# Kernel optimization log

Measured on AMD Instinct MI355X. Metric: run time of the kernel, lower is better.

## Reference

```python
import jax, jax.numpy as jnp
import numpy as np

STEPS = 100
RATE = 200
THR = 1.0
BETA = 0.0
SG_ALPHA = 2.0  # snntorch default ATan surrogate alpha


@jax.custom_vjp
def spike_fn(x):
    # heaviside spike with atan surrogate gradient (snntorch default)
    return (x > 0).astype(x.dtype)

def _spike_fwd(x):
    return spike_fn(x), x

def _spike_bwd(x, g):
    grad = (SG_ALPHA / 2.0) / (1.0 + (jnp.pi / 2.0 * SG_ALPHA * x) ** 2)
    return (g * grad,)

spike_fn.defvjp(_spike_fwd, _spike_bwd)


def conv2d(x, w):
    # x: [B,C,H,W], w: [O,I,K,K], VALID, stride 1, no bias
    return jax.lax.conv_general_dilated(
        x, w, window_strides=(1, 1), padding='VALID',
        dimension_numbers=('NCHW', 'OIHW', 'NCHW'))


def avg_pool2(x):
    s = jax.lax.reduce_window(x, 0.0, jax.lax.add, (1, 1, 2, 2), (1, 1, 2, 2), 'VALID')
    return s * 0.25


def lif(cur, mem):
    # snntorch Leaky, reset_mechanism='subtract'; reset signal is detached
    reset = jax.lax.stop_gradient((mem > THR).astype(cur.dtype))
    mem = BETA * mem + cur - reset * THR
    spk = spike_fn(mem - THR)
    return spk, mem


def setup_inputs() -> dict:
    key = jax.random.key(0)
    k1, k2, k3, k4 = jax.random.split(key, 4)
    B, C, H, W = 64, 3, 32, 32
    x = jax.random.uniform(k1, (B, C, H, W), dtype=jnp.float32)
    # kaiming-uniform-ish init scales (exact values irrelevant for correctness baseline)
    W_in = jax.random.normal(k2, (32, 3, 5, 5), dtype=jnp.float32) * 0.1
    W_h1 = jax.random.normal(k3, (64, 32, 5, 5), dtype=jnp.float32) * 0.05
    W_h2 = jax.random.normal(k4, (10, 1600), dtype=jnp.float32) * 0.02
    return {"x": x, "W_in": W_in, "W_h1": W_h1, "W_h2": W_h2}


def reference(x, W_in, W_h1, W_h2):
    B, C, H, W = x.shape
    K = W_in.shape[2]
    # poisson spike train: [steps, B, C, H, W]
    rescale = RATE / STEPS
    rand = jax.random.uniform(jax.random.key(1), (STEPS, B, C, H, W), dtype=x.dtype)
    spikes = (rand < x * rescale).astype(x.dtype)

    H1 = (H - K + 1) // 2; W1 = (W - K + 1) // 2           # after conv1+pool
    H2 = (H1 - K + 1) // 2; W2 = (W1 - K + 1) // 2          # after conv2+pool
    mem0 = (jnp.zeros((B, W_in.shape[0], H1, W1), x.dtype),
            jnp.zeros((B, W_h1.shape[0], H2, W2), x.dtype),
            jnp.zeros((B, W_h2.shape[0]), x.dtype))

    def step(carry, s):
        memin, memh1, memh2 = carry
        spkin, memin = lif(avg_pool2(conv2d(s, W_in)), memin)
        spkh1, memh1 = lif(avg_pool2(conv2d(spkin, W_h1)), memh1)
        flat = spkh1.reshape(spkh1.shape[0], -1)
        spkh2, memh2 = lif(flat @ W_h2.T, memh2)
        return (memin, memh1, memh2), (spkh2, memh2)

    _, (out_spikes, memh2_mem) = jax.lax.scan(step, mem0, spikes)
    return out_spikes, memh2_mem
```

## Files before the change

### kernel.cpp

```cpp
#include <hip/hip_runtime.h>
#include <stdint.h>


#define NSTEPS 100
#define NB 64
#define CAPF1 524288u
#define CAPF2 262144u

typedef short bf16x8 __attribute__((ext_vector_type(8)));
typedef float f32x4 __attribute__((ext_vector_type(4)));

__device__ __forceinline__ uint32_t rotl32(uint32_t v, uint32_t r) {
  return (v << r) | (v >> (32u - r));
}

__device__ __forceinline__ void threefry2x32(uint32_t k0, uint32_t k1,
                                             uint32_t& x0, uint32_t& x1) {
  uint32_t k2 = k0 ^ k1 ^ 0x1BD11BDAu;
  x0 += k0; x1 += k1;
#define TF_R(r) { x0 += x1; x1 = rotl32(x1, r); x1 ^= x0; }
  TF_R(13u) TF_R(15u) TF_R(26u) TF_R(6u)
  x0 += k1; x1 += k2 + 1u;
  TF_R(17u) TF_R(29u) TF_R(16u) TF_R(24u)
  x0 += k2; x1 += k0 + 2u;
  TF_R(13u) TF_R(15u) TF_R(26u) TF_R(6u)
  x0 += k0; x1 += k1 + 3u;
  TF_R(17u) TF_R(29u) TF_R(16u) TF_R(24u)
  x0 += k1; x1 += k2 + 4u;
  TF_R(13u) TF_R(15u) TF_R(26u) TF_R(6u)
  x0 += k2; x1 += k0 + 5u;
#undef TF_R
}

__device__ __forceinline__ double fold_pool_w(const float* W, int base, int pos) {
  int iy = pos / 6, ix = pos % 6;
  double w = 0.0;
  for (int dy = 0; dy < 2; ++dy) {
    int ky = iy - dy; if (ky < 0 || ky > 4) continue;
    for (int dx = 0; dx < 2; ++dx) {
      int kx = ix - dx; if (kx < 0 || kx > 4) continue;
      w += (double)W[base + ky * 5 + kx];
    }
  }
  return w;
}

__device__ __forceinline__ uint16_t f2bf(float x) {
  uint32_t u = __float_as_uint(x);
  uint32_t r = (u + 0x7fffu + ((u >> 16) & 1u)) >> 16;
  return (uint16_t)r;
}

__global__ __launch_bounds__(256) void prep_gen(const float* __restrict__ W_in,
                                                const float* __restrict__ W_h1,
                                                const float* __restrict__ x,
                                                double* __restrict__ W1R,
                                                double* __restrict__ W2R,
                                                uint16_t* __restrict__ WB1,
                                                uint16_t* __restrict__ WB2,
                                                float* __restrict__ EPS,
                                                uint32_t* __restrict__ cnt,
                                                uint32_t* __restrict__ rowm) {
  if (blockIdx.x >= 678) {
    int id = (blockIdx.x - 678) * 4 + (threadIdx.x >> 6);
    int lane = threadIdx.x & 63;
    int rp = id & 15, c = (id >> 4) % 3, tb = id / 48;
    int pix = rp * 64 + lane;
    int b = tb & 63;
    uint32_t i = (uint32_t)((tb * 3 + c) * 1024 + pix);
    uint32_t x0 = 0u, x1 = i;
    threefry2x32(0u, 1u, x0, x1);
    uint32_t bits = x0 ^ x1;
    float u = __uint_as_float((bits >> 9) | 0x3f800000u) - 1.0f;
    float xv = x[(b * 3 + c) * 1024 + pix];
    unsigned long long mask = __ballot(u < 2.0f * xv);
    if (lane == 0) ((unsigned long long*)rowm)[id] = mask;
    return;
  }
  if (blockIdx.x < 654) {
    int e = blockIdx.x * 256 + threadIdx.x;
    if (e < 3456) {
      int oj = e & 7, c = (e >> 3) % 3, pos = ((e >> 3) / 3) % 36, og = (e >> 3) / 108;
      int oc = og * 8 + oj;
      W1R[e] = fold_pool_w(W_in, (oc * 3 + c) * 25, pos);
    } else if (e < 77184) {
      int e2 = e - 3456;
      int oj = e2 & 15, pos = (e2 >> 4) % 36, c = ((e2 >> 4) / 36) % 32, og = e2 / 18432;
      int oc = og * 16 + oj;
      W2R[e2] = fold_pool_w(W_h1, (oc * 32 + c) * 25, pos);
    } else if (e < 93568) {
      int e3 = e - 77184;
      int j = e3 & 7, lane = (e3 >> 3) & 63, nt = (e3 >> 9) & 1, ks = (e3 >> 10) & 3, hl = e3 >> 12;
      int k = ks * 32 + (lane >> 4) * 8 + j;
      int oc = nt * 16 + (lane & 15);
      uint16_t val = 0;
      if (k < 108) {
        int c = k / 36, pos = k % 36;
        double w = fold_pool_w(W_in, (oc * 3 + c) * 25, pos);
        uint16_t hi = f2bf((float)w);
        if (hl == 0) val = hi;
        else {
          float hif = __uint_as_float(((uint32_t)hi) << 16);
          val = f2bf((float)(w - (double)hif));
        }
      }
      WB1[e3] = val;
    } else if (e < 167296) {
      int e4 = e - 93568;
      int j = e4 & 7, lane = (e4 >> 3) & 63, nt = (e4 >> 9) & 3, pos = e4 >> 11;
      int oc = nt * 16 + (lane & 15);
      int c  = (lane >> 4) * 8 + j;
      double w = fold_pool_w(W_h1, (oc * 32 + c) * 25, pos);
      uint16_t hi = f2bf((float)w);
      float hif = __uint_as_float(((uint32_t)hi) << 16);
      uint16_t lo = f2bf((float)(w - (double)hif));
      WB2[e4] = hi;
      WB2[73728 + e4] = lo;
    } else if (e < 167298) {
      cnt[e - 167296] = 0;
    }
  } else {
    int wid = threadIdx.x >> 6, lane = threadIdx.x & 63;
    int o = (blockIdx.x - 654) * 4 + wid;
    const double u24 = 5.9604644775390625e-08;
    double s = 0.0;
    if (o < 32) {
      for (int t = lane; t < 108; t += 64) {
        int pos = t / 3, c = t % 3;
        s += fabs(fold_pool_w(W_in, (o * 3 + c) * 25, pos));
      }
    } else {
      int oc = o - 32;
      for (int t = lane; t < 1152; t += 64) {
        int c = t / 36, pos = t % 36;
        s += fabs(fold_pool_w(W_h1, (oc * 32 + c) * 25, pos));
      }
    }
    #pragma unroll
    for (int off = 32; off > 0; off >>= 1) s += __shfl_xor(s, off);
    if (lane == 0)
      EPS[o] = (o < 32) ? (float)(s * (108.0 * u24 * 6.0) * 0.25)
                        : (float)(s * (1152.0 * u24 * 6.0) * 0.25);
  }
}

__global__ __launch_bounds__(256) void conv1_mfma(const uint32_t* __restrict__ rowm,
                                                  const uint16_t* __restrict__ WB1,
                                                  const float* __restrict__ EPS,
                                                  uint32_t* __restrict__ A1w,
                                                  uint32_t* __restrict__ B1w,
                                                  uint32_t* __restrict__ cnt,
                                                  uint32_t* __restrict__ list1) {
  __shared__ uint32_t sR[4][96];
  const int tid = threadIdx.x;
  const int wid = tid >> 6, lane = tid & 63;
  const int tb = blockIdx.x * 4 + wid;
  const int q = lane >> 4, ln = lane & 15;

  for (int i = lane; i < 96; i += 64) sR[wid][i] = rowm[tb * 96 + i];

  const float eps0 = EPS[ln];
  const float eps1 = EPS[16 + ln];

  bf16x8 bf[2][4][2];
  #pragma unroll
  for (int hl = 0; hl < 2; ++hl)
    #pragma unroll
    for (int ks = 0; ks < 4; ++ks)
      #pragma unroll
      for (int nt = 0; nt < 2; ++nt)
        bf[hl][ks][nt] =
            *(const bf16x8*)(WB1 + ((((hl * 4 + ks) * 2 + nt) * 64 + lane) * 8));

  const int wl = lane;
  const int qq = wl >> 2, rr = wl & 3;

  for (int mt = 0; mt < 13; ++mt) {
    int p = mt * 16 + ln;
    int pc = p < 196 ? p : 195;
    int oh = pc / 14, ow = pc % 14;
    uint64_t seg0 = 0, seg1 = 0, seg2 = 0;
    #pragma unroll
    for (int iy = 0; iy < 6; ++iy) {
      seg0 |= (uint64_t)((sR[wid][0 * 32 + 2 * oh + iy] >> (2 * ow)) & 0x3fu) << (6 * iy);
      seg1 |= (uint64_t)((sR[wid][1 * 32 + 2 * oh + iy] >> (2 * ow)) & 0x3fu) << (6 * iy);
      seg2 |= (uint64_t)((sR[wid][2 * 32 + 2 * oh + iy] >> (2 * ow)) & 0x3fu) << (6 * iy);
    }
    uint64_t lo = seg0 | (seg1 << 36);
    uint64_t hi = (seg1 >> 28) | (seg2 << 8);
    uint32_t wz[4] = {(uint32_t)lo, (uint32_t)(lo >> 32),
                      (uint32_t)hi, (uint32_t)(hi >> 32)};

    f32x4 acc0 = (f32x4)(0.0f), acc1 = (f32x4)(0.0f);
    #pragma unroll
    for (int ks = 0; ks < 4; ++ks) {
      uint32_t byte = (wz[ks] >> (q * 8)) & 0xffu;
      union { uint32_t u[4]; bf16x8 v; } a;
      #pragma unroll
      for (int i = 0; i < 4; ++i)
        a.u[i] = (((byte >> (2 * i)) & 1u) ? 0x3F80u : 0u) |
                 (((byte >> (2 * i + 1)) & 1u) ? 0x3F800000u : 0u);
      acc0 = __builtin_amdgcn_mfma_f32_16x16x32_bf16(a.v, bf[0][ks][0], acc0, 0, 0, 0);
      acc0 = __builtin_amdgcn_mfma_f32_16x16x32_bf16(a.v, bf[1][ks][0], acc0, 0, 0, 0);
      acc1 = __builtin_amdgcn_mfma_f32_16x16x32_bf16(a.v, bf[0][ks][1], acc1, 0, 0, 0);
      acc1 = __builtin_amdgcn_mfma_f32_16x16x32_bf16(a.v, bf[1][ks][1], acc1, 0, 0, 0);
    }

    unsigned long long bA0[4], bA1[4], bB0[4], bB1[4], bF0[4], bF1[4];
    #pragma unroll
    for (int r = 0; r < 4; ++r) {
      float c0 = acc0[r] * 0.25f;
      float c1 = acc1[r] * 0.25f;
      bA0[r] = __ballot(c0 > 1.0f);
      bB0[r] = __ballot(c0 > 2.0f);
      bF0[r] = __ballot(fabsf(c0 - 1.0f) <= eps0 || fabsf(c0 - 2.0f) <= eps0);
      bA1[r] = __ballot(c1 > 1.0f);
      bB1[r] = __ballot(c1 > 2.0f);
      bF1[r] = __ballot(fabsf(c1 - 1.0f) <= eps1 || fabsf(c1 - 2.0f) <= eps1);
    }

    int pw = mt * 16 + wl;
    if (wl < 16 && pw < 196) {
#define SEL(B) (rr == 0 ? B[0] : rr == 1 ? B[1] : rr == 2 ? B[2] : B[3])
      uint32_t wA = (uint32_t)((SEL(bA0) >> (qq * 16)) & 0xffffull) |
                    ((uint32_t)((SEL(bA1) >> (qq * 16)) & 0xffffull) << 16);
      uint32_t wB = (uint32_t)((SEL(bB0) >> (qq * 16)) & 0xffffull) |
                    ((uint32_t)((SEL(bB1) >> (qq * 16)) & 0xffffull) << 16);
      uint32_t wF = (uint32_t)((SEL(bF0) >> (qq * 16)) & 0xffffull) |
                    ((uint32_t)((SEL(bF1) >> (qq * 16)) & 0xffffull) << 16);
#undef SEL
      uint32_t idx = (uint32_t)(tb * 196 + pw);
      A1w[idx] = wA;
      B1w[idx] = wB;
      if (wF) {
        uint32_t n = (uint32_t)__popc(wF);
        uint32_t slot = atomicAdd(&cnt[0], n);
        uint32_t base = idx * 32u;
        while (wF) {
          int bit = __ffs(wF) - 1; wF &= wF - 1;
          if (slot < CAPF1) list1[slot] = base + (uint32_t)bit;
          ++slot;
        }
      }
    }
  }
}

__global__ __launch_bounds__(256) void fix1c(const uint32_t* __restrict__ cnt,
                                             const uint32_t* __restrict__ list,
                                             const uint32_t* __restrict__ rowm,
                                             const double* __restrict__ W1R,
                                             uint32_t* __restrict__ A1w,
                                             uint32_t* __restrict__ B1w) {
  uint32_t total = cnt[0]; if (total > CAPF1) total = CAPF1;
  const uint32_t g = blockIdx.x * 32 + (threadIdx.x >> 3);
  const int l = threadIdx.x & 7;
  const uint32_t gstride = gridDim.x * 32;
  for (uint32_t i = g; i < total; i += gstride) {
    uint32_t e = list[i];
    uint32_t x = e >> 5;
    int oc = (int)(e & 31u);
    int tb = (int)(x / 196), p = (int)(x % 196);
    int oh = p / 14, ow = p % 14;
    int og = oc >> 3, oj = oc & 7;
    const uint32_t* R = rowm + (size_t)tb * 96;
    double acc = 0.0;
    for (int t = l; t < 108; t += 8) {
      int pos = t / 3, c = t - pos * 3;
      int iy = pos / 6, ix = pos - iy * 6;
      double bd = (double)((R[c * 32 + 2 * oh + iy] >> (2 * ow + ix)) & 1u);
      acc = fma(bd, W1R[og * 864 + pos * 24 + c * 8 + oj], acc);
    }
    acc += __shfl_xor(acc, 1);
    acc += __shfl_xor(acc, 2);
    acc += __shfl_xor(acc, 4);
    if (l == 0) {
      float cur = (float)(acc * 0.25);
      uint32_t m = 1u << oc;
      if (cur > 1.0f) atomicOr(&A1w[x], m); else atomicAnd(&A1w[x], ~m);
      if (cur > 2.0f) atomicOr(&B1w[x], m); else atomicAnd(&B1w[x], ~m);
    }
  }
}

__global__ __launch_bounds__(64) void scan1(const uint32_t* __restrict__ A1w,
                                            const uint32_t* __restrict__ B1w,
                                            uint32_t* __restrict__ mask1) {
  int chain = blockIdx.x * 64 + threadIdx.x;
  if (chain >= NB * 196) return;
  int b = chain / 196, p = chain % 196;
  const size_t stride = (size_t)NB * 196;
  size_t base = (size_t)b * 196 + p;
  uint32_t prev = 0;
  #pragma unroll
  for (int seg = 0; seg < 4; ++seg) {
    uint32_t Abuf[25], Bbuf[25];
    size_t sb = base + (size_t)(seg * 25) * stride;
    #pragma unroll
    for (int i = 0; i < 25; ++i) {
      Abuf[i] = A1w[sb + i * stride];
      Bbuf[i] = B1w[sb + i * stride];
    }
    #pragma unroll
    for (int i = 0; i < 25; ++i) {
      uint32_t s = (Abuf[i] & ~prev) | (Bbuf[i] & prev);
      mask1[sb + i * stride] = s;
      prev = s;
    }
  }
}

#define CONV2_EPILOG(ACC, TBV)                                                \
  {                                                                           \
    const int w = lane;                                                       \
    const int pw = w >> 1, hfw = w & 1;                                       \
    _Pragma("unroll")                                                         \
    for (int mt2 = 0; mt2 < 2; ++mt2) {                                       \
      const int pt = pw - mt2 * 16;                                           \
      const bool wvalid = (w < 50) && (pt >= 0) && (pt < 16) && (pw < 25);    \
      const int qw = (pt & 15) >> 2, rw = pt & 3;                             \
      uint32_t wA = 0, wB = 0, wF = 0;                                        \
      _Pragma("unroll")                                                       \
      for (int nt = 0; nt < 4; ++nt) {                                        \
        unsigned long long bA[4], bB[4], bF[4];                               \
        _Pragma("unroll")                                                     \
        for (int reg = 0; reg < 4; ++reg) {                                   \
          float c = ACC[mt2 * 4 + nt][reg] * 0.25f;                           \
          float e = epsv[nt];                                                 \
          bA[reg] = __ballot(c > 1.0f);                                       \
          bB[reg] = __ballot(c > 2.0f);                                       \
          bF[reg] = __ballot(fabsf(c - 1.0f) <= e || fabsf(c - 2.0f) <= e);   \
        }                                                                     \
        if (wvalid && (nt >> 1) == hfw) {                                     \
          const int sh = (nt & 1) * 16;                                       \
          unsigned long long sA = rw == 0 ? bA[0] : rw == 1 ? bA[1] : rw == 2 ? bA[2] : bA[3]; \
          unsigned long long sB = rw == 0 ? bB[0] : rw == 1 ? bB[1] : rw == 2 ? bB[2] : bB[3]; \
          unsigned long long sF = rw == 0 ? bF[0] : rw == 1 ? bF[1] : rw == 2 ? bF[2] : bF[3]; \
          wA |= (uint32_t)((sA >> (qw * 16)) & 0xffffull) << sh;              \
          wB |= (uint32_t)((sB >> (qw * 16)) & 0xffffull) << sh;              \
          wF |= (uint32_t)((sF >> (qw * 16)) & 0xffffull) << sh;              \
        }                                                                     \
      }                                                                       \
      if (wvalid) {                                                           \
        uint32_t idx = (uint32_t)((TBV) * 25 + pw) * 2 + hfw;                 \
        A2w[idx] = wA;                                                        \
        B2w[idx] = wB;                                                        \
        if (wF) {                                                             \
          uint32_t n = (uint32_t)__popc(wF);                                  \
          uint32_t slot = atomicAdd(&cnt[1], n);                              \
          uint32_t base2 = idx * 32u;                                         \
          while (wF) {                                                        \
            int bit = __ffs(wF) - 1; wF &= wF - 1;                            \
            if (slot < CAPF2) list2[slot] = base2 + (uint32_t)bit;            \
            ++slot;                                                           \
          }                                                                   \
        }                                                                     \
      }                                                                       \
    }                                                                         \
  }

__global__ __launch_bounds__(256, 3) void conv2_mfma(const uint32_t* __restrict__ mask1,
                                                     const uint16_t* __restrict__ WB,
                                                     const float* __restrict__ EPS,
                                                     uint32_t* __restrict__ A2w,
                                                     uint32_t* __restrict__ B2w,
                                                     uint32_t* __restrict__ cnt,
                                                     uint32_t* __restrict__ list2) {
  __shared__ uint32_t sM[8 * 196];
  const int tid = threadIdx.x;
  const int wid = tid >> 6, lane = tid & 63;
  const int tb0 = blockIdx.x * 8 + wid * 2;

  for (int i = lane; i < 392; i += 64)
    sM[wid * 392 + i] = mask1[(size_t)tb0 * 196 + i];

  const int q  = lane >> 4;
  const int ln = lane & 15;
  float epsv[4];
  #pragma unroll
  for (int nt = 0; nt < 4; ++nt) epsv[nt] = EPS[32 + nt * 16 + ln];

  const int p0 = ln;
  const int p1 = 16 + ln;
  const bool v1 = (p1 < 25);
  const int oh0 = p0 / 5, ow0 = p0 % 5;
  const int p1c = v1 ? p1 : 0;
  const int oh1 = p1c / 5, ow1 = p1c % 5;

  f32x4 accA[8], accB[8];
  #pragma unroll
  for (int i = 0; i < 8; ++i) { accA[i] = (f32x4)(0.0f); accB[i] = (f32x4)(0.0f); }

  const uint32_t* sW0 = &sM[wid * 392];
  const uint32_t* sW1 = sW0 + 196;

  for (int iy = 0; iy < 6; ++iy) {
    #pragma unroll
    for (int ix = 0; ix < 6; ++ix) {
      const int pos = iy * 6 + ix;
      const int o0 = (2 * oh0 + iy) * 14 + 2 * ow0 + ix;
      const int o1 = (2 * oh1 + iy) * 14 + 2 * ow1 + ix;
      uint32_t w00 = sW0[o0];
      uint32_t w01 = v1 ? sW0[o1] : 0u;
      uint32_t w10 = sW1[o0];
      uint32_t w11 = v1 ? sW1[o1] : 0u;
      uint32_t b00 = (w00 >> (q * 8)) & 0xffu;
      uint32_t b01 = (w01 >> (q * 8)) & 0xffu;
      uint32_t b10 = (w10 >> (q * 8)) & 0xffu;
      uint32_t b11 = (w11 >> (q * 8)) & 0xffu;
      union { uint32_t u[4]; bf16x8 v; } a00, a01, a10, a11;
      #pragma unroll
      for (int i = 0; i < 4; ++i) {
        a00.u[i] = (((b00 >> (2 * i)) & 1u) ? 0x3F80u : 0u) |
                   (((b00 >> (2 * i + 1)) & 1u) ? 0x3F800000u : 0u);
        a01.u[i] = (((b01 >> (2 * i)) & 1u) ? 0x3F80u : 0u) |
                   (((b01 >> (2 * i + 1)) & 1u) ? 0x3F800000u : 0u);
        a10.u[i] = (((b10 >> (2 * i)) & 1u) ? 0x3F80u : 0u) |
                   (((b10 >> (2 * i + 1)) & 1u) ? 0x3F800000u : 0u);
        a11.u[i] = (((b11 >> (2 * i)) & 1u) ? 0x3F80u : 0u) |
                   (((b11 >> (2 * i + 1)) & 1u) ? 0x3F800000u : 0u);
      }
      const uint16_t* bhi_base = WB + (size_t)pos * 2048 + lane * 8;
      const uint16_t* blo_base = bhi_base + 73728;
      #pragma unroll
      for (int nt = 0; nt < 4; ++nt) {
        bf16x8 bhi = *(const bf16x8*)(bhi_base + nt * 512);
        bf16x8 blo = *(const bf16x8*)(blo_base + nt * 512);
        accA[nt] = __builtin_amdgcn_mfma_f32_16x16x32_bf16(a00.v, bhi, accA[nt], 0, 0, 0);
        accA[nt] = __builtin_amdgcn_mfma_f32_16x16x32_bf16(a00.v, blo, accA[nt], 0, 0, 0);
        accA[4 + nt] = __builtin_amdgcn_mfma_f32_16x16x32_bf16(a01.v, bhi, accA[4 + nt], 0, 0, 0);
        accA[4 + nt] = __builtin_amdgcn_mfma_f32_16x16x32_bf16(a01.v, blo, accA[4 + nt], 0, 0, 0);
        accB[nt] = __builtin_amdgcn_mfma_f32_16x16x32_bf16(a10.v, bhi, accB[nt], 0, 0, 0);
        accB[nt] = __builtin_amdgcn_mfma_f32_16x16x32_bf16(a10.v, blo, accB[nt], 0, 0, 0);
        accB[4 + nt] = __builtin_amdgcn_mfma_f32_16x16x32_bf16(a11.v, bhi, accB[4 + nt], 0, 0, 0);
        accB[4 + nt] = __builtin_amdgcn_mfma_f32_16x16x32_bf16(a11.v, blo, accB[4 + nt], 0, 0, 0);
      }
    }
  }

  CONV2_EPILOG(accA, tb0)
  CONV2_EPILOG(accB, (tb0 + 1))
}

__global__ __launch_bounds__(256) void fix2c(const uint32_t* __restrict__ cnt,
                                             const uint32_t* __restrict__ list,
                                             const uint32_t* __restrict__ mask1,
                                             const double* __restrict__ W2R,
                                             uint32_t* __restrict__ A2w,
                                             uint32_t* __restrict__ B2w) {
  uint32_t total = cnt[1]; if (total > CAPF2) total = CAPF2;
  const uint32_t g = blockIdx.x * 16 + (threadIdx.x >> 4);
  const int l = threadIdx.x & 15;
  const uint32_t gstride = gridDim.x * 16;
  for (uint32_t i = g; i < total; i += gstride) {
    uint32_t e = list[i];
    uint32_t wi = e >> 5;
    int bit = (int)(e & 31u);
    uint32_t x = wi >> 1;
    int oc = (int)((wi & 1u) * 32u) + bit;
    int tb = (int)(x / 25), p = (int)(x % 25);
    int oh = p / 5, ow = p % 5;
    int og = oc >> 4, oj = oc & 15;
    const uint32_t* M = mask1 + (size_t)tb * 196;
    double acc = 0.0;
    for (int t = l; t < 1152; t += 16) {
      int c = t / 36, pos = t - c * 36;
      int iy = pos / 6, ix = pos - iy * 6;
      uint32_t mm = M[(2 * oh + iy) * 14 + 2 * ow + ix];
      double bd = (double)((mm >> c) & 1u);
      acc = fma(bd, W2R[og * 18432 + c * 576 + pos * 16 + oj], acc);
    }
    acc += __shfl_xor(acc, 1);
    acc += __shfl_xor(acc, 2);
    acc += __shfl_xor(acc, 4);
    acc += __shfl_xor(acc, 8);
    if (l == 0) {
      float cur = (float)(acc * 0.25);
      uint32_t m = 1u << bit;
      if (cur > 1.0f) atomicOr(&A2w[wi], m); else atomicAnd(&A2w[wi], ~m);
      if (cur > 2.0f) atomicOr(&B2w[wi], m); else atomicAnd(&B2w[wi], ~m);
    }
  }
}

__global__ __launch_bounds__(64) void scan2(const uint64_t* __restrict__ A2q,
                                            const uint64_t* __restrict__ B2q,
                                            uint64_t* __restrict__ mask2) {
  int chain = blockIdx.x * 64 + threadIdx.x;
  if (chain >= NB * 25) return;
  int b = chain / 25, p = chain % 25;
  const size_t stride = (size_t)NB * 25;
  size_t base = (size_t)b * 25 + p;
  uint64_t prev = 0;
  #pragma unroll
  for (int seg = 0; seg < 4; ++seg) {
    uint64_t Abuf[25], Bbuf[25];
    size_t sb = base + (size_t)(seg * 25) * stride;
    #pragma unroll
    for (int i = 0; i < 25; ++i) {
      Abuf[i] = A2q[sb + i * stride];
      Bbuf[i] = B2q[sb + i * stride];
    }
    #pragma unroll
    for (int i = 0; i < 25; ++i) {
      uint64_t s = (Abuf[i] & ~prev) | (Bbuf[i] & prev);
      mask2[sb + i * stride] = s;
      prev = s;
    }
  }
}

__global__ __launch_bounds__(256) void fc_kernel(const uint64_t* __restrict__ mask2,
                                                 const float* __restrict__ W2,
                                                 float* __restrict__ cur3) {
  int gid = blockIdx.x * 256 + threadIdx.x;
  if (gid >= NSTEPS * NB * 80) return;
  int tb = gid / 80, r = gid % 80;
  int o = r >> 3, s = r & 7;
  const uint64_t* m = mask2 + (size_t)tb * 25;
  const float* w = W2 + o * 1600 + s * 200;

  uint64_t mw[25];
  #pragma unroll
  for (int p = 0; p < 25; ++p) mw[p] = m[p];

  const int oc0 = s * 8;
  double acc0 = 0.0, acc1 = 0.0;
  #pragma unroll
  for (int j = 0; j < 8; ++j) {
    const float* wj = w + j * 25;
    double a = 0.0;
    #pragma unroll
    for (int p = 0; p < 25; ++p) {
      double bd = (double)((mw[p] >> (oc0 + j)) & 1ull);
      a = fma(bd, (double)wj[p], a);
    }
    if (j & 1) acc1 += a; else acc0 += a;
  }
  double acc = acc0 + acc1;
  acc += __shfl_xor(acc, 4);
  acc += __shfl_xor(acc, 2);
  acc += __shfl_xor(acc, 1);
  if (s == 0) cur3[tb * 10 + o] = (float)acc;
}

__global__ __launch_bounds__(64) void lif3_kernel(const float* __restrict__ cur3,
                                                  float* __restrict__ out) {
  int bo = blockIdx.x * 64 + threadIdx.x;
  if (bo >= NB * 10) return;
  float prev = 0.0f;
  #pragma unroll
  for (int seg = 0; seg < 4; ++seg) {
    float cbuf[25];
    #pragma unroll
    for (int i = 0; i < 25; ++i) cbuf[i] = cur3[(seg * 25 + i) * 640 + bo];
    #pragma unroll
    for (int i = 0; i < 25; ++i) {
      int t = seg * 25 + i;
      float mem = cbuf[i] - prev;
      bool s = mem > 1.0f;
      out[t * 640 + bo] = s ? 1.0f : 0.0f;
      out[NSTEPS * 640 + t * 640 + bo] = mem;
      prev = s ? 1.0f : 0.0f;
    }
  }
}

extern "C" void kernel_launch(void* const* d_in, const int* in_sizes, int n_in,
                              void* d_out, int out_size, void* d_ws, size_t ws_size,
                              hipStream_t stream) {
  const float* x    = (const float*)d_in[0];
  const float* W_in = (const float*)d_in[1];
  const float* W_h1 = (const float*)d_in[2];
  const float* W_h2 = (const float*)d_in[3];
  float* out = (float*)d_out;

  unsigned char* ws = (unsigned char*)d_ws;
  double*   W1R   = (double*)(ws + 0);
  double*   W2R   = (double*)(ws + 27648);
  uint16_t* WB1   = (uint16_t*)(ws + 617472);
  uint16_t* WB2   = (uint16_t*)(ws + 650240);
  float*    EPS   = (float*)(ws + 945152);
  uint32_t* cnt   = (uint32_t*)(ws + 945536);
  uint32_t* rowm  = (uint32_t*)(ws + 945664);
  uint32_t* A1w   = (uint32_t*)(ws + 3403264);
  uint32_t* B1w   = (uint32_t*)(ws + 8420864);
  uint32_t* mask1 = (uint32_t*)(ws + 13438464);
  uint32_t* A2w   = (uint32_t*)(ws + 18456064);
  uint32_t* B2w   = (uint32_t*)(ws + 19736064);
  uint64_t* mask2 = (uint64_t*)(ws + 21016064);
  float*    cur3  = (float*)(ws + 22296064);
  uint32_t* list1 = (uint32_t*)(ws + 22552064);
  uint32_t* list2 = (uint32_t*)(ws + 24649216);

  prep_gen<<<678 + 76800, 256, 0, stream>>>(W_in, W_h1, x, W1R, W2R, WB1, WB2,
                                            EPS, cnt, rowm);
  conv1_mfma<<<1600, 256, 0, stream>>>(rowm, WB1, EPS, A1w, B1w, cnt, list1);
  fix1c<<<1024, 256, 0, stream>>>(cnt, list1, rowm, W1R, A1w, B1w);
  scan1<<<(NB * 196 + 63) / 64, 64, 0, stream>>>(A1w, B1w, mask1);
  conv2_mfma<<<800, 256, 0, stream>>>(mask1, WB2, EPS, A2w, B2w, cnt, list2);
  fix2c<<<1024, 256, 0, stream>>>(cnt, list2, mask1, W2R, A2w, B2w);
  scan2<<<(NB * 25 + 63) / 64, 64, 0, stream>>>((const uint64_t*)A2w,
                                                (const uint64_t*)B2w, mask2);
  fc_kernel<<<(NSTEPS * NB * 80 + 255) / 256, 256, 0, stream>>>(mask2, W_h2, cur3);
  lif3_kernel<<<10, 64, 0, stream>>>(cur3, out);
}
```

Before: 299.3 us.

## Fuse borderline-threshold fp64 recheck into conv1 and conv2 epilogues, drop fix kernels

Conv outputs that land near a spike threshold used to be appended to global lists with atomics and recomputed in fp64 by two separate fix kernels. That recheck now runs inside the conv1 and conv2 epilogues: the wave walks the flagged bits one at a time and recomputes each value in fp64 from the mask data it already holds. This removes two kernel launches, the atomic counter and list traffic, and the atomic read-modify-write on the bitmasks. The cost is that the whole wave serialises over each flagged element, which can stretch the conv kernels if many values are flagged.

```diff
diff --git a/kernel.cpp b/kernel.cpp
--- a/kernel.cpp
+++ b/kernel.cpp
@@ -4,8 +4,6 @@
 
 #define NSTEPS 100
 #define NB 64
-#define CAPF1 524288u
-#define CAPF2 262144u
 
 typedef short bf16x8 __attribute__((ext_vector_type(8)));
 typedef float f32x4 __attribute__((ext_vector_type(4)));
@@ -59,7 +57,6 @@
                                                 uint16_t* __restrict__ WB1,
                                                 uint16_t* __restrict__ WB2,
                                                 float* __restrict__ EPS,
-                                                uint32_t* __restrict__ cnt,
                                                 uint32_t* __restrict__ rowm) {
   if (blockIdx.x >= 678) {
     int id = (blockIdx.x - 678) * 4 + (threadIdx.x >> 6);
@@ -116,8 +113,6 @@
       uint16_t lo = f2bf((float)(w - (double)hif));
       WB2[e4] = hi;
       WB2[73728 + e4] = lo;
-    } else if (e < 167298) {
-      cnt[e - 167296] = 0;
     }
   } else {
     int wid = threadIdx.x >> 6, lane = threadIdx.x & 63;
@@ -147,10 +142,9 @@
 __global__ __launch_bounds__(256) void conv1_mfma(const uint32_t* __restrict__ rowm,
                                                   const uint16_t* __restrict__ WB1,
                                                   const float* __restrict__ EPS,
+                                                  const double* __restrict__ W1R,
                                                   uint32_t* __restrict__ A1w,
-                                                  uint32_t* __restrict__ B1w,
-                                                  uint32_t* __restrict__ cnt,
-                                                  uint32_t* __restrict__ list1) {
+                                                  uint32_t* __restrict__ B1w) {
   __shared__ uint32_t sR[4][96];
   const int tid = threadIdx.x;
   const int wid = tid >> 6, lane = tid & 63;
@@ -220,65 +214,50 @@
     }
 
     int pw = mt * 16 + wl;
-    if (wl < 16 && pw < 196) {
+    const bool wvalid = (wl < 16 && pw < 196);
+    uint32_t wA = 0, wB = 0, wF = 0;
+    if (wvalid) {
 #define SEL(B) (rr == 0 ? B[0] : rr == 1 ? B[1] : rr == 2 ? B[2] : B[3])
-      uint32_t wA = (uint32_t)((SEL(bA0) >> (qq * 16)) & 0xffffull) |
-                    ((uint32_t)((SEL(bA1) >> (qq * 16)) & 0xffffull) << 16);
-      uint32_t wB = (uint32_t)((SEL(bB0) >> (qq * 16)) & 0xffffull) |
-                    ((uint32_t)((SEL(bB1) >> (qq * 16)) & 0xffffull) << 16);
-      uint32_t wF = (uint32_t)((SEL(bF0) >> (qq * 16)) & 0xffffull) |
-                    ((uint32_t)((SEL(bF1) >> (qq * 16)) & 0xffffull) << 16);
+      wA = (uint32_t)((SEL(bA0) >> (qq * 16)) & 0xffffull) |
+           ((uint32_t)((SEL(bA1) >> (qq * 16)) & 0xffffull) << 16);
+      wB = (uint32_t)((SEL(bB0) >> (qq * 16)) & 0xffffull) |
+           ((uint32_t)((SEL(bB1) >> (qq * 16)) & 0xffffull) << 16);
+      wF = (uint32_t)((SEL(bF0) >> (qq * 16)) & 0xffffull) |
+           ((uint32_t)((SEL(bF1) >> (qq * 16)) & 0xffffull) << 16);
 #undef SEL
+    }
+
+    unsigned long long flagged = __ballot(wF != 0);
+    while (flagged) {
+      int src = (int)__ffsll(flagged) - 1;
+      uint32_t fsrc = (uint32_t)__shfl((int)wF, src);
+      int ocb = __ffs((int)fsrc) - 1;
+      int pf = mt * 16 + src;
+      int ohf = pf / 14, owf = pf % 14;
+      int og = ocb >> 3, oj = ocb & 7;
+      double acc = 0.0;
+      for (int t = lane; t < 108; t += 64) {
+        int pos = t / 3, c = t - pos * 3;
+        int iy = pos / 6, ix = pos - iy * 6;
+        double bd = (double)((sR[wid][c * 32 + 2 * ohf + iy] >> (2 * owf + ix)) & 1u);
+        acc = fma(bd, W1R[og * 864 + pos * 24 + c * 8 + oj], acc);
+      }
+      #pragma unroll
+      for (int off = 32; off > 0; off >>= 1) acc += __shfl_xor(acc, off);
+      float cur = (float)(acc * 0.25);
+      if (lane == src) {
+        uint32_t m = 1u << ocb;
+        wA = (cur > 1.0f) ? (wA | m) : (wA & ~m);
+        wB = (cur > 2.0f) ? (wB | m) : (wB & ~m);
+        wF &= wF - 1;
+      }
+      flagged = __ballot(wF != 0);
+    }
+
+    if (wvalid) {
       uint32_t idx = (uint32_t)(tb * 196 + pw);
       A1w[idx] = wA;
       B1w[idx] = wB;
-      if (wF) {
-        uint32_t n = (uint32_t)__popc(wF);
-        uint32_t slot = atomicAdd(&cnt[0], n);
-        uint32_t base = idx * 32u;
-        while (wF) {
-          int bit = __ffs(wF) - 1; wF &= wF - 1;
-          if (slot < CAPF1) list1[slot] = base + (uint32_t)bit;
-          ++slot;
-        }
-      }
-    }
-  }
-}
-
-__global__ __launch_bounds__(256) void fix1c(const uint32_t* __restrict__ cnt,
-                                             const uint32_t* __restrict__ list,
-                                             const uint32_t* __restrict__ rowm,
-                                             const double* __restrict__ W1R,
-                                             uint32_t* __restrict__ A1w,
-                                             uint32_t* __restrict__ B1w) {
-  uint32_t total = cnt[0]; if (total > CAPF1) total = CAPF1;
-  const uint32_t g = blockIdx.x * 32 + (threadIdx.x >> 3);
-  const int l = threadIdx.x & 7;
-  const uint32_t gstride = gridDim.x * 32;
-  for (uint32_t i = g; i < total; i += gstride) {
-    uint32_t e = list[i];
-    uint32_t x = e >> 5;
-    int oc = (int)(e & 31u);
-    int tb = (int)(x / 196), p = (int)(x % 196);
-    int oh = p / 14, ow = p % 14;
-    int og = oc >> 3, oj = oc & 7;
-    const uint32_t* R = rowm + (size_t)tb * 96;
-    double acc = 0.0;
-    for (int t = l; t < 108; t += 8) {
-      int pos = t / 3, c = t - pos * 3;
-      int iy = pos / 6, ix = pos - iy * 6;
-      double bd = (double)((R[c * 32 + 2 * oh + iy] >> (2 * ow + ix)) & 1u);
-      acc = fma(bd, W1R[og * 864 + pos * 24 + c * 8 + oj], acc);
-    }
-    acc += __shfl_xor(acc, 1);
-    acc += __shfl_xor(acc, 2);
-    acc += __shfl_xor(acc, 4);
-    if (l == 0) {
-      float cur = (float)(acc * 0.25);
-      uint32_t m = 1u << oc;
-      if (cur > 1.0f) atomicOr(&A1w[x], m); else atomicAnd(&A1w[x], ~m);
-      if (cur > 2.0f) atomicOr(&B1w[x], m); else atomicAnd(&B1w[x], ~m);
     }
   }
 }
@@ -310,62 +289,86 @@
   }
 }
 
-#define CONV2_EPILOG(ACC, TBV)                                                \
-  {                                                                           \
-    const int w = lane;                                                       \
-    const int pw = w >> 1, hfw = w & 1;                                       \
-    _Pragma("unroll")                                                         \
-    for (int mt2 = 0; mt2 < 2; ++mt2) {                                       \
-      const int pt = pw - mt2 * 16;                                           \
-      const bool wvalid = (w < 50) && (pt >= 0) && (pt < 16) && (pw < 25);    \
-      const int qw = (pt & 15) >> 2, rw = pt & 3;                             \
-      uint32_t wA = 0, wB = 0, wF = 0;                                        \
-      _Pragma("unroll")                                                       \
-      for (int nt = 0; nt < 4; ++nt) {                                        \
-        unsigned long long bA[4], bB[4], bF[4];                               \
-        _Pragma("unroll")                                                     \
-        for (int reg = 0; reg < 4; ++reg) {                                   \
-          float c = ACC[mt2 * 4 + nt][reg] * 0.25f;                           \
-          float e = epsv[nt];                                                 \
-          bA[reg] = __ballot(c > 1.0f);                                       \
-          bB[reg] = __ballot(c > 2.0f);                                       \
-          bF[reg] = __ballot(fabsf(c - 1.0f) <= e || fabsf(c - 2.0f) <= e);   \
-        }                                                                     \
-        if (wvalid && (nt >> 1) == hfw) {                                     \
-          const int sh = (nt & 1) * 16;                                       \
-          unsigned long long sA = rw == 0 ? bA[0] : rw == 1 ? bA[1] : rw == 2 ? bA[2] : bA[3]; \
-          unsigned long long sB = rw == 0 ? bB[0] : rw == 1 ? bB[1] : rw == 2 ? bB[2] : bB[3]; \
-          unsigned long long sF = rw == 0 ? bF[0] : rw == 1 ? bF[1] : rw == 2 ? bF[2] : bF[3]; \
-          wA |= (uint32_t)((sA >> (qw * 16)) & 0xffffull) << sh;              \
-          wB |= (uint32_t)((sB >> (qw * 16)) & 0xffffull) << sh;              \
-          wF |= (uint32_t)((sF >> (qw * 16)) & 0xffffull) << sh;              \
-        }                                                                     \
-      }                                                                       \
-      if (wvalid) {                                                           \
-        uint32_t idx = (uint32_t)((TBV) * 25 + pw) * 2 + hfw;                 \
-        A2w[idx] = wA;                                                        \
-        B2w[idx] = wB;                                                        \
-        if (wF) {                                                             \
-          uint32_t n = (uint32_t)__popc(wF);                                  \
-          uint32_t slot = atomicAdd(&cnt[1], n);                              \
-          uint32_t base2 = idx * 32u;                                         \
-          while (wF) {                                                        \
-            int bit = __ffs(wF) - 1; wF &= wF - 1;                            \
-            if (slot < CAPF2) list2[slot] = base2 + (uint32_t)bit;            \
-            ++slot;                                                           \
-          }                                                                   \
-        }                                                                     \
-      }                                                                       \
-    }                                                                         \
-  }
+__device__ __forceinline__ void conv2_epilog(const f32x4* ACC, int TBV,
+                                             const uint32_t* SW,
+                                             const float* epsv,
+                                             const double* __restrict__ W2R,
+                                             uint32_t* __restrict__ A2w,
+                                             uint32_t* __restrict__ B2w,
+                                             int lane) {
+  const int w = lane;
+  const int pw = w >> 1, hfw = w & 1;
+  #pragma unroll
+  for (int mt2 = 0; mt2 < 2; ++mt2) {
+    const int pt = pw - mt2 * 16;
+    const bool wvalid = (w < 50) && (pt >= 0) && (pt < 16) && (pw < 25);
+    const int qw = (pt & 15) >> 2, rw = pt & 3;
+    uint32_t wA = 0, wB = 0, wF = 0;
+    #pragma unroll
+    for (int nt = 0; nt < 4; ++nt) {
+      unsigned long long bA[4], bB[4], bF[4];
+      #pragma unroll
+      for (int reg = 0; reg < 4; ++reg) {
+        float c = ACC[mt2 * 4 + nt][reg] * 0.25f;
+        float e = epsv[nt];
+        bA[reg] = __ballot(c > 1.0f);
+        bB[reg] = __ballot(c > 2.0f);
+        bF[reg] = __ballot(fabsf(c - 1.0f) <= e || fabsf(c - 2.0f) <= e);
+      }
+      if (wvalid && (nt >> 1) == hfw) {
+        const int sh = (nt & 1) * 16;
+        unsigned long long sA = rw == 0 ? bA[0] : rw == 1 ? bA[1] : rw == 2 ? bA[2] : bA[3];
+        unsigned long long sB = rw == 0 ? bB[0] : rw == 1 ? bB[1] : rw == 2 ? bB[2] : bB[3];
+        unsigned long long sF = rw == 0 ? bF[0] : rw == 1 ? bF[1] : rw == 2 ? bF[2] : bF[3];
+        wA |= (uint32_t)((sA >> (qw * 16)) & 0xffffull) << sh;
+        wB |= (uint32_t)((sB >> (qw * 16)) & 0xffffull) << sh;
+        wF |= (uint32_t)((sF >> (qw * 16)) & 0xffffull) << sh;
+      }
+    }
+
+    unsigned long long flagged = __ballot(wF != 0);
+    while (flagged) {
+      int src = (int)__ffsll(flagged) - 1;
+      uint32_t fsrc = (uint32_t)__shfl((int)wF, src);
+      int bit = __ffs((int)fsrc) - 1;
+      int psrc = src >> 1, hfs = src & 1;
+      int oc = hfs * 32 + bit;
+      int ohf = psrc / 5, owf = psrc % 5;
+      int og = oc >> 4, oj = oc & 15;
+      double acc = 0.0;
+      for (int t = lane; t < 1152; t += 64) {
+        int c = t / 36, pos = t - c * 36;
+        int iy = pos / 6, ix = pos - iy * 6;
+        uint32_t mm = SW[(2 * ohf + iy) * 14 + 2 * owf + ix];
+        acc = fma((double)((mm >> c) & 1u),
+                  W2R[og * 18432 + c * 576 + pos * 16 + oj], acc);
+      }
+      #pragma unroll
+      for (int off = 32; off > 0; off >>= 1) acc += __shfl_xor(acc, off);
+      float cur = (float)(acc * 0.25);
+      if (lane == src) {
+        uint32_t m = 1u << bit;
+        wA = (cur > 1.0f) ? (wA | m) : (wA & ~m);
+        wB = (cur > 2.0f) ? (wB | m) : (wB & ~m);
+        wF &= wF - 1;
+      }
+      flagged = __ballot(wF != 0);
+    }
+
+    if (wvalid) {
+      uint32_t idx = (uint32_t)(TBV * 25 + pw) * 2 + hfw;
+      A2w[idx] = wA;
+      B2w[idx] = wB;
+    }
+  }
+}
 
 __global__ __launch_bounds__(256, 3) void conv2_mfma(const uint32_t* __restrict__ mask1,
                                                      const uint16_t* __restrict__ WB,
                                                      const float* __restrict__ EPS,
+                                                     const double* __restrict__ W2R,
                                                      uint32_t* __restrict__ A2w,
-                                                     uint32_t* __restrict__ B2w,
-                                                     uint32_t* __restrict__ cnt,
-                                                     uint32_t* __restrict__ list2) {
+                                                     uint32_t* __restrict__ B2w) {
   __shared__ uint32_t sM[8 * 196];
   const int tid = threadIdx.x;
   const int wid = tid >> 6, lane = tid & 63;
@@ -438,49 +441,8 @@
     }
   }
 
-  CONV2_EPILOG(accA, tb0)
-  CONV2_EPILOG(accB, (tb0 + 1))
-}
-
-__global__ __launch_bounds__(256) void fix2c(const uint32_t* __restrict__ cnt,
-                                             const uint32_t* __restrict__ list,
-                                             const uint32_t* __restrict__ mask1,
-                                             const double* __restrict__ W2R,
-                                             uint32_t* __restrict__ A2w,
-                                             uint32_t* __restrict__ B2w) {
-  uint32_t total = cnt[1]; if (total > CAPF2) total = CAPF2;
-  const uint32_t g = blockIdx.x * 16 + (threadIdx.x >> 4);
-  const int l = threadIdx.x & 15;
-  const uint32_t gstride = gridDim.x * 16;
-  for (uint32_t i = g; i < total; i += gstride) {
-    uint32_t e = list[i];
-    uint32_t wi = e >> 5;
-    int bit = (int)(e & 31u);
-    uint32_t x = wi >> 1;
-    int oc = (int)((wi & 1u) * 32u) + bit;
-    int tb = (int)(x / 25), p = (int)(x % 25);
-    int oh = p / 5, ow = p % 5;
-    int og = oc >> 4, oj = oc & 15;
-    const uint32_t* M = mask1 + (size_t)tb * 196;
-    double acc = 0.0;
-    for (int t = l; t < 1152; t += 16) {
-      int c = t / 36, pos = t - c * 36;
-      int iy = pos / 6, ix = pos - iy * 6;
-      uint32_t mm = M[(2 * oh + iy) * 14 + 2 * ow + ix];
-      double bd = (double)((mm >> c) & 1u);
-      acc = fma(bd, W2R[og * 18432 + c * 576 + pos * 16 + oj], acc);
-    }
-    acc += __shfl_xor(acc, 1);
-    acc += __shfl_xor(acc, 2);
-    acc += __shfl_xor(acc, 4);
-    acc += __shfl_xor(acc, 8);
-    if (l == 0) {
-      float cur = (float)(acc * 0.25);
-      uint32_t m = 1u << bit;
-      if (cur > 1.0f) atomicOr(&A2w[wi], m); else atomicAnd(&A2w[wi], ~m);
-      if (cur > 2.0f) atomicOr(&B2w[wi], m); else atomicAnd(&B2w[wi], ~m);
-    }
-  }
+  conv2_epilog(accA, tb0,     sW0, epsv, W2R, A2w, B2w, lane);
+  conv2_epilog(accB, tb0 + 1, sW1, epsv, W2R, A2w, B2w, lane);
 }
 
 __global__ __launch_bounds__(64) void scan2(const uint64_t* __restrict__ A2q,
@@ -581,7 +543,6 @@
   uint16_t* WB1   = (uint16_t*)(ws + 617472);
   uint16_t* WB2   = (uint16_t*)(ws + 650240);
   float*    EPS   = (float*)(ws + 945152);
-  uint32_t* cnt   = (uint32_t*)(ws + 945536);
   uint32_t* rowm  = (uint32_t*)(ws + 945664);
   uint32_t* A1w   = (uint32_t*)(ws + 3403264);
   uint32_t* B1w   = (uint32_t*)(ws + 8420864);
@@ -590,16 +551,12 @@
   uint32_t* B2w   = (uint32_t*)(ws + 19736064);
   uint64_t* mask2 = (uint64_t*)(ws + 21016064);
   float*    cur3  = (float*)(ws + 22296064);
-  uint32_t* list1 = (uint32_t*)(ws + 22552064);
-  uint32_t* list2 = (uint32_t*)(ws + 24649216);
 
   prep_gen<<<678 + 76800, 256, 0, stream>>>(W_in, W_h1, x, W1R, W2R, WB1, WB2,
-                                            EPS, cnt, rowm);
-  conv1_mfma<<<1600, 256, 0, stream>>>(rowm, WB1, EPS, A1w, B1w, cnt, list1);
-  fix1c<<<1024, 256, 0, stream>>>(cnt, list1, rowm, W1R, A1w, B1w);
+                                            EPS, rowm);
+  conv1_mfma<<<1600, 256, 0, stream>>>(rowm, WB1, EPS, W1R, A1w, B1w);
   scan1<<<(NB * 196 + 63) / 64, 64, 0, stream>>>(A1w, B1w, mask1);
-  conv2_mfma<<<800, 256, 0, stream>>>(mask1, WB2, EPS, A2w, B2w, cnt, list2);
-  fix2c<<<1024, 256, 0, stream>>>(cnt, list2, mask1, W2R, A2w, B2w);
+  conv2_mfma<<<800, 256, 0, stream>>>(mask1, WB2, EPS, W2R, A2w, B2w);
   scan2<<<(NB * 25 + 63) / 64, 64, 0, stream>>>((const uint64_t*)A2w,
                                                 (const uint64_t*)B2w, mask2);
   fc_kernel<<<(NSTEPS * NB * 80 + 255) / 256, 256, 0, stream>>>(mask2, W_h2, cur3);
```

After: 288.4 us. -3.6%, faster.
